# Kernel optimization log

Hardware: AMD Instinct MI355X
Metric: run time of the kernel (lower is better)

Reference implementation:

```python
import jax, jax.numpy as jnp
import numpy as np
from jax import lax

WINDOW_SIZE = 11
C1 = 0.01 ** 2
C2 = 0.03 ** 2


def make_window(window_size: int) -> jnp.ndarray:
    # scipy.ndimage.gaussian_filter(np.ones(ws), sigma) with mode='reflect'
    # preserves constant inputs exactly, so gauss_1d == ones(ws).
    # outer(ones, ones) / sum -> uniform box window of weight 1/ws^2.
    return jnp.full((window_size, window_size), 1.0 / (window_size * window_size), dtype=jnp.float32)


def setup_inputs() -> dict:
    key = jax.random.key(0)
    k1, k2 = jax.random.split(key)
    B, C, D, H, W = 1, 1, 64, 512, 512
    x = jax.random.uniform(k1, (B, C, D, H, W), dtype=jnp.float32)
    y = jax.random.uniform(k2, (B, C, D, H, W), dtype=jnp.float32)
    window = make_window(WINDOW_SIZE)
    return {"x": x, "y": y, "window": window}


def _windowed_sum(imgs, window):
    # imgs: [N,1,H,W]; window: [ws,ws]. 'same' cross-correlation (window is symmetric).
    ws = window.shape[0]
    pad = ws // 2
    w = window[None, None, :, :]  # [O=1, I=1, ws, ws]
    return lax.conv_general_dilated(
        imgs, w, window_strides=(1, 1), padding=[(pad, pad), (pad, pad)],
        dimension_numbers=("NCHW", "OIHW", "NCHW"))


def reference(x, y, window):
    B, C, D, H, W = x.shape
    # Fold depth into the conv batch dim: every depth slice is an independent 2D SSIM.
    xs = x.transpose(0, 2, 1, 3, 4).reshape(B * D, C, H, W)
    ys = y.transpose(0, 2, 1, 3, 4).reshape(B * D, C, H, W)
    # Single batched conv over [x, y, x^2, y^2, x*y]
    stacked = jnp.concatenate([xs, ys, xs * xs, ys * ys, xs * ys], axis=0)
    conv = _windowed_sum(stacked, window)
    mu_x, mu_y, e_x2, e_y2, e_xy = jnp.split(conv, 5, axis=0)
    mu_x_sq = mu_x * mu_x
    mu_y_sq = mu_y * mu_y
    mu_xy = mu_x * mu_y
    sigma_x_sq = e_x2 - mu_x_sq
    sigma_y_sq = e_y2 - mu_y_sq
    sigma_xy = e_xy - mu_xy
    ssim_map = ((2.0 * mu_xy + C1) * (2.0 * sigma_xy + C2)) / (
        (mu_x_sq + mu_y_sq + C1) * (sigma_x_sq + sigma_y_sq + C2))
    # Per-slice means averaged over slices == global mean (all slices same size).
    return 1.0 - ssim_map.mean()
```

## Files before the change

kernel.cpp:

```cpp
#include <hip/hip_runtime.h>


constexpr int IMG    = 512;
constexpr int OUT_R  = 22;
constexpr int CHUNKS = (IMG + OUT_R - 1) / OUT_R;
constexpr int ITERS  = (OUT_R + 10) / 4;
constexpr int PW     = 524;
constexpr int PLANE  = 4 * PW;
constexpr float WSCALE = 1.0f / 121.0f;
constexpr float C1F = 1e-4f;
constexpr float C2F = 9e-4f;

__device__ __forceinline__ int sidx(int c) {
  return c ^ (((c >> 5) & 3) << 1);
}

template <bool ATOMIC>
__global__ __launch_bounds__(256, 3) void ssim_main(const float* __restrict__ x,
                                                    const float* __restrict__ y,
                                                    float* __restrict__ out_ws) {
  __shared__ float slab[5 * PLANE];
  __shared__ float wsum[4];

  const int tid   = threadIdx.x;
  const int chunk = blockIdx.x;
  const int z     = blockIdx.y;
  const int O0    = chunk * OUT_R;
  const int r0    = O0 - 5;
  const float* xs = x + (size_t)z * IMG * IMG;
  const float* ys = y + (size_t)z * IMG * IMG;

  if (tid < 240) {
    const int q  = tid / 48;
    const int rj = (tid % 48) / 12;
    const int ci = tid % 12;
    const int c  = (ci < 6) ? ci : (518 + ci - 6);
    slab[q * PLANE + rj * PW + sidx(c)] = 0.f;
  }

  const int c0 = 2 * tid;
  float sX0 = 0.f, sX1 = 0.f, sY0 = 0.f, sY1 = 0.f;
  float sXX0 = 0.f, sXX1 = 0.f, sYY0 = 0.f, sYY1 = 0.f, sXY0 = 0.f, sXY1 = 0.f;

  const int wb = sidx(c0 + 6);

  const int g    = tid & 63;
  const int jrow = tid >> 6;
  int ra[10];
#pragma unroll
  for (int m = 0; m < 10; ++m) ra[m] = jrow * PW + sidx(8 * g + 2 * m);

  float acc = 0.f;

  for (int k = 0; k < ITERS; ++k) {
#pragma unroll
    for (int j = 0; j < 4; ++j) {
      const int gr = r0 + 4 * k + j;
      float2 xn = make_float2(0.f, 0.f), yn = make_float2(0.f, 0.f);
      float2 xo = make_float2(0.f, 0.f), yo = make_float2(0.f, 0.f);
      if ((unsigned)gr < (unsigned)IMG) {
        xn = *(const float2*)(xs + (size_t)gr * IMG + c0);
        yn = *(const float2*)(ys + (size_t)gr * IMG + c0);
      }
      const int gro = gr - 11;
      if (gro >= r0 && (unsigned)gro < (unsigned)IMG) {
        xo = *(const float2*)(xs + (size_t)gro * IMG + c0);
        yo = *(const float2*)(ys + (size_t)gro * IMG + c0);
      }
      sX0  += xn.x - xo.x;               sX1  += xn.y - xo.y;
      sY0  += yn.x - yo.x;               sY1  += yn.y - yo.y;
      sXX0 += xn.x * xn.x - xo.x * xo.x; sXX1 += xn.y * xn.y - xo.y * xo.y;
      sYY0 += yn.x * yn.x - yo.x * yo.x; sYY1 += yn.y * yn.y - yo.y * yo.y;
      sXY0 += xn.x * yn.x - xo.x * yo.x; sXY1 += xn.y * yn.y - xo.y * yo.y;

      *(float2*)&slab[0 * PLANE + j * PW + wb] = make_float2(sX0, sX1);
      *(float2*)&slab[1 * PLANE + j * PW + wb] = make_float2(sY0, sY1);
      *(float2*)&slab[2 * PLANE + j * PW + wb] = make_float2(sXX0, sXX1);
      *(float2*)&slab[3 * PLANE + j * PW + wb] = make_float2(sYY0, sYY1);
      *(float2*)&slab[4 * PLANE + j * PW + wb] = make_float2(sXY0, sXY1);
    }
    __syncthreads();

    const int iw   = 4 * k + jrow;
    const int orow = O0 + iw - 10;
    if (iw >= 10 && orow < IMG) {
      float b[5][8];
#pragma unroll
      for (int q = 0; q < 5; ++q) {
        float v[20];
#pragma unroll
        for (int m = 0; m < 10; ++m) {
          const float2 t = *(const float2*)&slab[q * PLANE + ra[m]];
          v[2 * m] = t.x; v[2 * m + 1] = t.y;
        }
        float s = v[1];
#pragma unroll
        for (int k2 = 2; k2 <= 11; ++k2) s += v[k2];
        b[q][0] = s;
#pragma unroll
        for (int j2 = 1; j2 < 8; ++j2) { s += v[j2 + 11] - v[j2]; b[q][j2] = s; }
      }
#pragma unroll
      for (int j2 = 0; j2 < 8; ++j2) {
        const float mu_x = b[0][j2] * WSCALE;
        const float mu_y = b[1][j2] * WSCALE;
        const float ex2  = b[2][j2] * WSCALE;
        const float ey2  = b[3][j2] * WSCALE;
        const float exy  = b[4][j2] * WSCALE;
        const float mxx = mu_x * mu_x;
        const float myy = mu_y * mu_y;
        const float mxy = mu_x * mu_y;
        const float num = fmaf(2.f, mxy, C1F) * fmaf(2.f, exy - mxy, C2F);
        const float den = (mxx + myy + C1F) * ((ex2 - mxx) + (ey2 - myy) + C2F);
        acc += num * __builtin_amdgcn_rcpf(den);
      }
    }
    __syncthreads();
  }

#pragma unroll
  for (int off = 32; off > 0; off >>= 1) acc += __shfl_down(acc, off, 64);
  if ((tid & 63) == 0) wsum[tid >> 6] = acc;
  __syncthreads();
  if (tid == 0) {
    const float t = wsum[0] + wsum[1] + wsum[2] + wsum[3];
    if (ATOMIC) {
      atomicAdd(out_ws, t);
    } else {
      out_ws[blockIdx.y * CHUNKS + blockIdx.x] = t;
    }
  }
}

__global__ void ssim_finalize(const float* __restrict__ partials, int n,
                              float* __restrict__ out) {
  __shared__ float wsum[4];
  float acc = 0.f;
  for (int i = threadIdx.x; i < n; i += 256) acc += partials[i];
#pragma unroll
  for (int off = 32; off > 0; off >>= 1) acc += __shfl_down(acc, off, 64);
  if ((threadIdx.x & 63) == 0) wsum[threadIdx.x >> 6] = acc;
  __syncthreads();
  if (threadIdx.x == 0) {
    const float t = wsum[0] + wsum[1] + wsum[2] + wsum[3];
    out[0] = 1.0f - t * (1.0f / (64.0f * 512.0f * 512.0f));
  }
}

__global__ void ssim_zero(float* p) {
  if (threadIdx.x == 0) p[0] = 0.f;
}

__global__ void ssim_finalize_atomic(const float* __restrict__ accp,
                                     float* __restrict__ out) {
  if (threadIdx.x == 0)
    out[0] = 1.0f - accp[0] * (1.0f / (64.0f * 512.0f * 512.0f));
}

extern "C" void kernel_launch(void* const* d_in, const int* in_sizes, int n_in,
                              void* d_out, int out_size, void* d_ws, size_t ws_size,
                              hipStream_t stream) {
  const float* x = (const float*)d_in[0];
  const float* y = (const float*)d_in[1];
  float* out = (float*)d_out;

  dim3 grid(CHUNKS, 64);
  dim3 block(256);
  const int nblocks = CHUNKS * 64;

  if (ws_size >= (size_t)nblocks * sizeof(float)) {
    float* partials = (float*)d_ws;
    ssim_main<false><<<grid, block, 0, stream>>>(x, y, partials);
    ssim_finalize<<<1, 256, 0, stream>>>(partials, nblocks, out);
  } else {
    float* accp = (float*)d_ws;
    ssim_zero<<<1, 64, 0, stream>>>(accp);
    ssim_main<true><<<grid, block, 0, stream>>>(x, y, accp);
    ssim_finalize_atomic<<<1, 64, 0, stream>>>(accp, out);
  }
}
```

Baseline: 184.3 us.

## Replace LDS slab with per-wave register sliding window and bpermute horizontal sums

Each wave now owns a 16-row band and holds 8 columns per lane in registers, keeping the vertical running sums in registers. Horizontal box sums are built from neighbouring lanes with ds_bpermute, so the shared-memory slab and block-wide barriers are gone. Block indices are remapped so blocks that share an XCD work on the same depth slices, and the next rows are prefetched with double-buffered loads. The cost is higher register pressure (launch bounds drop to 2 blocks per CU) and more redundant halo row reads per band (26 input rows for 16 output rows).

```diff
diff --git a/kernel.cpp b/kernel.cpp
--- a/kernel.cpp
+++ b/kernel.cpp
@@ -1,112 +1,121 @@
 #include <hip/hip_runtime.h>
 
 
-constexpr int IMG    = 512;
-constexpr int OUT_R  = 22;
-constexpr int CHUNKS = (IMG + OUT_R - 1) / OUT_R;
-constexpr int ITERS  = (OUT_R + 10) / 4;
-constexpr int PW     = 524;
-constexpr int PLANE  = 4 * PW;
+constexpr int IMG   = 512;
+constexpr int RB    = 16;
+constexpr int BANDS = IMG / RB;
+constexpr int WPB   = 4;
+constexpr int NBLK  = 64 * BANDS / WPB;
 constexpr float WSCALE = 1.0f / 121.0f;
 constexpr float C1F = 1e-4f;
 constexpr float C2F = 9e-4f;
 
-__device__ __forceinline__ int sidx(int c) {
-  return c ^ (((c >> 5) & 3) << 1);
+__device__ __forceinline__ float bperm(int addr, float v) {
+  return __int_as_float(__builtin_amdgcn_ds_bpermute(addr, __float_as_int(v)));
 }
 
 template <bool ATOMIC>
-__global__ __launch_bounds__(256, 3) void ssim_main(const float* __restrict__ x,
+__global__ __launch_bounds__(256, 2) void ssim_main(const float* __restrict__ x,
                                                     const float* __restrict__ y,
                                                     float* __restrict__ out_ws) {
-  __shared__ float slab[5 * PLANE];
-  __shared__ float wsum[4];
-
-  const int tid   = threadIdx.x;
-  const int chunk = blockIdx.x;
-  const int z     = blockIdx.y;
-  const int O0    = chunk * OUT_R;
-  const int r0    = O0 - 5;
-  const float* xs = x + (size_t)z * IMG * IMG;
-  const float* ys = y + (size_t)z * IMG * IMG;
-
-  if (tid < 240) {
-    const int q  = tid / 48;
-    const int rj = (tid % 48) / 12;
-    const int ci = tid % 12;
-    const int c  = (ci < 6) ? ci : (518 + ci - 6);
-    slab[q * PLANE + rj * PW + sidx(c)] = 0.f;
-  }
-
-  const int c0 = 2 * tid;
-  float sX0 = 0.f, sX1 = 0.f, sY0 = 0.f, sY1 = 0.f;
-  float sXX0 = 0.f, sXX1 = 0.f, sYY0 = 0.f, sYY1 = 0.f, sXY0 = 0.f, sXY1 = 0.f;
-
-  const int wb = sidx(c0 + 6);
-
-  const int g    = tid & 63;
-  const int jrow = tid >> 6;
-  int ra[10];
-#pragma unroll
-  for (int m = 0; m < 10; ++m) ra[m] = jrow * PW + sidx(8 * g + 2 * m);
-
+  __shared__ float wsum[WPB];
+
+  const int tid  = threadIdx.x;
+  const int lane = tid & 63;
+  const int wid  = tid >> 6;
+
+  const int bid  = blockIdx.x;
+  const int xcd  = bid & 7;
+  const int qq   = bid >> 3;
+  const int z    = xcd * 8 + (qq >> 3);
+  const int band = (qq & 7) * WPB + wid;
+  const int o0   = band * RB;
+  const int gs   = o0 - 5;
+
+  const float* xs = x + (size_t)z * IMG * IMG + lane * 8;
+  const float* ys = y + (size_t)z * IMG * IMG + lane * 8;
+
+  const int addrL = ((lane + 63) & 63) << 2;
+  const int addrR = ((lane + 1) & 63) << 2;
+  const bool l0  = (lane == 0);
+  const bool l63 = (lane == 63);
+
+  float sX[8] = {}, sY[8] = {}, sXX[8] = {}, sYY[8] = {}, sXY[8] = {};
+  float cxA[8], cyA[8], oxA[8], oyA[8];
+  float cxB[8], cyB[8], oxB[8], oyB[8];
   float acc = 0.f;
 
-  for (int k = 0; k < ITERS; ++k) {
-#pragma unroll
-    for (int j = 0; j < 4; ++j) {
-      const int gr = r0 + 4 * k + j;
-      float2 xn = make_float2(0.f, 0.f), yn = make_float2(0.f, 0.f);
-      float2 xo = make_float2(0.f, 0.f), yo = make_float2(0.f, 0.f);
-      if ((unsigned)gr < (unsigned)IMG) {
-        xn = *(const float2*)(xs + (size_t)gr * IMG + c0);
-        yn = *(const float2*)(ys + (size_t)gr * IMG + c0);
+  auto ldrow8 = [&](const float* p, bool valid, float (&d)[8]) {
+    if (valid) {
+      const float4 a = *(const float4*)p;
+      const float4 b = *(const float4*)(p + 4);
+      d[0] = a.x; d[1] = a.y; d[2] = a.z; d[3] = a.w;
+      d[4] = b.x; d[5] = b.y; d[6] = b.z; d[7] = b.w;
+    } else {
+#pragma unroll
+      for (int j = 0; j < 8; ++j) d[j] = 0.f;
+    }
+  };
+
+  auto hwin = [&](const float (&S)[8], float (&B)[8]) {
+    float vm5 = bperm(addrL, S[3]);
+    float vm4 = bperm(addrL, S[4]);
+    float vm3 = bperm(addrL, S[5]);
+    float vm2 = bperm(addrL, S[6]);
+    float vm1 = bperm(addrL, S[7]);
+    float vp8  = bperm(addrR, S[0]);
+    float vp9  = bperm(addrR, S[1]);
+    float vp10 = bperm(addrR, S[2]);
+    float vp11 = bperm(addrR, S[3]);
+    float vp12 = bperm(addrR, S[4]);
+    vm5  = l0  ? 0.f : vm5;   vm4  = l0  ? 0.f : vm4;
+    vm3  = l0  ? 0.f : vm3;   vm2  = l0  ? 0.f : vm2;
+    vm1  = l0  ? 0.f : vm1;
+    vp8  = l63 ? 0.f : vp8;   vp9  = l63 ? 0.f : vp9;
+    vp10 = l63 ? 0.f : vp10;  vp11 = l63 ? 0.f : vp11;
+    vp12 = l63 ? 0.f : vp12;
+    float s = (((vm5 + vm4) + (vm3 + vm2)) + ((vm1 + S[0]) + (S[1] + S[2]))) +
+              ((S[3] + S[4]) + S[5]);
+    B[0] = s;
+    s += S[6]  - vm5;  B[1] = s;
+    s += S[7]  - vm4;  B[2] = s;
+    s += vp8   - vm3;  B[3] = s;
+    s += vp9   - vm2;  B[4] = s;
+    s += vp10  - vm1;  B[5] = s;
+    s += vp11  - S[0]; B[6] = s;
+    s += vp12  - S[1]; B[7] = s;
+  };
+
+  auto step = [&](int i, bool steady,
+                  float (&cx)[8], float (&cy)[8], float (&ox)[8], float (&oy)[8],
+                  float (&nx)[8], float (&ny)[8], float (&px)[8], float (&py)[8]) {
+    const int gr = gs + i;
+    const bool nv = ((unsigned)(gr + 1) < (unsigned)IMG) && (i < RB + 9);
+    ldrow8(xs + (gr + 1) * IMG, nv, nx);
+    ldrow8(ys + (gr + 1) * IMG, nv, ny);
+
+    if (steady) {
+      const int gro = gr - 10;
+      const bool ov = (gro >= 0);
+      ldrow8(xs + gro * IMG, ov, px);
+      ldrow8(ys + gro * IMG, ov, py);
+#pragma unroll
+      for (int j = 0; j < 8; ++j) {
+        sX[j] += cx[j] - ox[j];
+        sY[j] += cy[j] - oy[j];
+        sXX[j] = fmaf(cx[j], cx[j], fmaf(-ox[j], ox[j], sXX[j]));
+        sYY[j] = fmaf(cy[j], cy[j], fmaf(-oy[j], oy[j], sYY[j]));
+        sXY[j] = fmaf(cx[j], cy[j], fmaf(-ox[j], oy[j], sXY[j]));
       }
-      const int gro = gr - 11;
-      if (gro >= r0 && (unsigned)gro < (unsigned)IMG) {
-        xo = *(const float2*)(xs + (size_t)gro * IMG + c0);
-        yo = *(const float2*)(ys + (size_t)gro * IMG + c0);
-      }
-      sX0  += xn.x - xo.x;               sX1  += xn.y - xo.y;
-      sY0  += yn.x - yo.x;               sY1  += yn.y - yo.y;
-      sXX0 += xn.x * xn.x - xo.x * xo.x; sXX1 += xn.y * xn.y - xo.y * xo.y;
-      sYY0 += yn.x * yn.x - yo.x * yo.x; sYY1 += yn.y * yn.y - yo.y * yo.y;
-      sXY0 += xn.x * yn.x - xo.x * yo.x; sXY1 += xn.y * yn.y - xo.y * yo.y;
-
-      *(float2*)&slab[0 * PLANE + j * PW + wb] = make_float2(sX0, sX1);
-      *(float2*)&slab[1 * PLANE + j * PW + wb] = make_float2(sY0, sY1);
-      *(float2*)&slab[2 * PLANE + j * PW + wb] = make_float2(sXX0, sXX1);
-      *(float2*)&slab[3 * PLANE + j * PW + wb] = make_float2(sYY0, sYY1);
-      *(float2*)&slab[4 * PLANE + j * PW + wb] = make_float2(sXY0, sXY1);
-    }
-    __syncthreads();
-
-    const int iw   = 4 * k + jrow;
-    const int orow = O0 + iw - 10;
-    if (iw >= 10 && orow < IMG) {
-      float b[5][8];
-#pragma unroll
-      for (int q = 0; q < 5; ++q) {
-        float v[20];
-#pragma unroll
-        for (int m = 0; m < 10; ++m) {
-          const float2 t = *(const float2*)&slab[q * PLANE + ra[m]];
-          v[2 * m] = t.x; v[2 * m + 1] = t.y;
-        }
-        float s = v[1];
-#pragma unroll
-        for (int k2 = 2; k2 <= 11; ++k2) s += v[k2];
-        b[q][0] = s;
-#pragma unroll
-        for (int j2 = 1; j2 < 8; ++j2) { s += v[j2 + 11] - v[j2]; b[q][j2] = s; }
-      }
-#pragma unroll
-      for (int j2 = 0; j2 < 8; ++j2) {
-        const float mu_x = b[0][j2] * WSCALE;
-        const float mu_y = b[1][j2] * WSCALE;
-        const float ex2  = b[2][j2] * WSCALE;
-        const float ey2  = b[3][j2] * WSCALE;
-        const float exy  = b[4][j2] * WSCALE;
+      float bX[8], bY[8], bXX[8], bYY[8], bXY[8];
+      hwin(sX, bX); hwin(sY, bY); hwin(sXX, bXX); hwin(sYY, bYY); hwin(sXY, bXY);
+#pragma unroll
+      for (int j = 0; j < 8; ++j) {
+        const float mu_x = bX[j] * WSCALE;
+        const float mu_y = bY[j] * WSCALE;
+        const float ex2  = bXX[j] * WSCALE;
+        const float ey2  = bYY[j] * WSCALE;
+        const float exy  = bXY[j] * WSCALE;
         const float mxx = mu_x * mu_x;
         const float myy = mu_y * mu_y;
         const float mxy = mu_x * mu_y;
@@ -114,20 +123,46 @@
         const float den = (mxx + myy + C1F) * ((ex2 - mxx) + (ey2 - myy) + C2F);
         acc += num * __builtin_amdgcn_rcpf(den);
       }
+    } else {
+#pragma unroll
+      for (int j = 0; j < 8; ++j) {
+        sX[j] += cx[j];
+        sY[j] += cy[j];
+        sXX[j] = fmaf(cx[j], cx[j], sXX[j]);
+        sYY[j] = fmaf(cy[j], cy[j], sYY[j]);
+        sXY[j] = fmaf(cx[j], cy[j], sXY[j]);
+      }
     }
-    __syncthreads();
+  };
+
+  ldrow8(xs + gs * IMG, gs >= 0, cxA);
+  ldrow8(ys + gs * IMG, gs >= 0, cyA);
+#pragma unroll
+  for (int j = 0; j < 8; ++j) {
+    oxA[j] = 0.f; oyA[j] = 0.f; oxB[j] = 0.f; oyB[j] = 0.f;
+  }
+
+#pragma unroll 1
+  for (int i = 0; i < 10; i += 2) {
+    step(i,     false, cxA, cyA, oxA, oyA, cxB, cyB, oxB, oyB);
+    step(i + 1, false, cxB, cyB, oxB, oyB, cxA, cyA, oxA, oyA);
+  }
+#pragma unroll 1
+  for (int i = 10; i < RB + 10; i += 2) {
+    step(i,     true, cxA, cyA, oxA, oyA, cxB, cyB, oxB, oyB);
+    step(i + 1, true, cxB, cyB, oxB, oyB, cxA, cyA, oxA, oyA);
   }
 
 #pragma unroll
   for (int off = 32; off > 0; off >>= 1) acc += __shfl_down(acc, off, 64);
-  if ((tid & 63) == 0) wsum[tid >> 6] = acc;
+  if (lane == 0) wsum[wid] = acc;
   __syncthreads();
   if (tid == 0) {
     const float t = wsum[0] + wsum[1] + wsum[2] + wsum[3];
     if (ATOMIC) {
       atomicAdd(out_ws, t);
     } else {
-      out_ws[blockIdx.y * CHUNKS + blockIdx.x] = t;
+      out_ws[bid] = t;
     }
   }
 }
@@ -164,14 +199,13 @@
   const float* y = (const float*)d_in[1];
   float* out = (float*)d_out;
 
-  dim3 grid(CHUNKS, 64);
+  dim3 grid(NBLK);
   dim3 block(256);
-  const int nblocks = CHUNKS * 64;
-
-  if (ws_size >= (size_t)nblocks * sizeof(float)) {
+
+  if (ws_size >= (size_t)NBLK * sizeof(float)) {
     float* partials = (float*)d_ws;
     ssim_main<false><<<grid, block, 0, stream>>>(x, y, partials);
-    ssim_finalize<<<1, 256, 0, stream>>>(partials, nblocks, out);
+    ssim_finalize<<<1, 256, 0, stream>>>(partials, NBLK, out);
   } else {
     float* accp = (float*)d_ws;
     ssim_zero<<<1, 64, 0, stream>>>(accp);
```

Result: faster. 172.7 us (-6.3%).
